# Optimization experiments

Hardware: AMD Instinct MI355X
Metric: run time of the kernel (lower is better)

The kernel has to match this reference:

```python
import jax, jax.numpy as jnp
import numpy as np

NEG_MASK = -9e15
ALPHA = 0.2  # LeakyReLU negative slope


def _gat_layer(h, adj, W, a):
    # h: [B,K,Fin], adj: [B,K,K], W: [Fin,F], a: [2F]
    Wh = jnp.einsum('bki,io->bko', h, W)            # [B,K,F]
    F = Wh.shape[-1]
    a_src, a_dst = a[:F], a[F:]
    # e_ij = LeakyReLU(a . [Wh_i || Wh_j]) = LeakyReLU(Wh_i.a_src + Wh_j.a_dst)
    f_src = Wh @ a_src                              # [B,K]
    f_dst = Wh @ a_dst                              # [B,K]
    e = jax.nn.leaky_relu(f_src[:, :, None] + f_dst[:, None, :], ALPHA)  # [B,K,K]
    e = jnp.where(adj > 0, e, NEG_MASK)
    att = jax.nn.softmax(e, axis=2)                 # softmax over neighbors j
    # dropout is identity in eval mode (training=False)
    h_prime = jnp.einsum('bkj,bjo->bko', att, Wh)   # [B,K,F]
    return jax.nn.elu(h_prime)


def setup_inputs() -> dict:
    key = jax.random.key(0)
    ks = jax.random.split(key, 6)
    B, K, Fin, H, Fout = 128, 512, 224, 64, 32
    x = jax.random.normal(ks[0], (B, K, Fin), dtype=jnp.float32)
    adj = jax.random.randint(ks[1], (B, K, K), 0, 2, dtype=jnp.int32)
    W1 = jax.random.normal(ks[2], (Fin, H), dtype=jnp.float32) * (1.0 / np.sqrt(Fin))
    a1 = jax.random.normal(ks[3], (2 * H,), dtype=jnp.float32) * 0.1
    W2 = jax.random.normal(ks[4], (H, Fout), dtype=jnp.float32) * (1.0 / np.sqrt(H))
    a2 = jax.random.normal(ks[5], (2 * Fout,), dtype=jnp.float32) * 0.1
    return {"x": x, "adj": adj, "W1": W1, "a1": a1, "W2": W2, "a2": a2}


def reference(x, adj, W1, a1, W2, a2):
    h = _gat_layer(x, adj, W1, a1)   # conv1: in -> hidden
    h = _gat_layer(h, adj, W2, a2)   # conv2: hidden -> out
    return h
```

## Files before the change

### kernel.cpp

```cpp
#include <hip/hip_runtime.h>
#include <stdint.h>


#define B_   128
#define K_   512
#define FIN  224
#define H1   64
#define H2   32

typedef float    f32x4 __attribute__((ext_vector_type(4)));
typedef short    s16x8 __attribute__((ext_vector_type(8)));
typedef unsigned short u16;

__device__ __forceinline__ u16 f2bf(float f){
  uint32_t u = __float_as_uint(f);
  u += 0x7FFFu + ((u >> 16) & 1u);
  return (u16)(u >> 16);
}
__device__ __forceinline__ float bf2f(u16 h){ return __uint_as_float(((uint32_t)h) << 16); }

__global__ __launch_bounds__(256) void k_bitmask(const int* __restrict__ adj, uint32_t* __restrict__ bits){
  size_t w = (size_t)blockIdx.x * 256 + threadIdx.x;
  const int4* p = reinterpret_cast<const int4*>(adj) + w * 8;
  uint32_t m = 0;
#pragma unroll
  for (int c = 0; c < 8; ++c){
    int4 v = p[c];
    m |= (v.x != 0 ? 1u : 0u) << (4*c + 0);
    m |= (v.y != 0 ? 1u : 0u) << (4*c + 1);
    m |= (v.z != 0 ? 1u : 0u) << (4*c + 2);
    m |= (v.w != 0 ? 1u : 0u) << (4*c + 3);
  }
  bits[w] = m;
}

__global__ __launch_bounds__(256) void k_prep(const float* __restrict__ W1, const float* __restrict__ W2,
                                              u16* __restrict__ W1b, u16* __restrict__ W2b){
  int t = blockIdx.x * 256 + threadIdx.x;
  if (t < FIN * H1) W1b[t] = f2bf(W1[t]);
  else { int u = t - FIN * H1; if (u < H1 * H2) W2b[u] = f2bf(W2[u]); }
}

template<int KD, int NO, bool AF32>
__global__ __launch_bounds__(256) void k_gemm(const void* __restrict__ Ain, const u16* __restrict__ Wb,
                                              const float* __restrict__ avec,
                                              u16* __restrict__ Whout, float* __restrict__ fs, float* __restrict__ fd){
  __shared__ u16 xs[64 * 40];
  __shared__ u16 wtT[NO * 56];
  const int tid  = threadIdx.x;
  const int wid  = tid >> 6, lane = tid & 63;
  const int g    = lane >> 4, lr = lane & 15;
  const size_t row0 = (size_t)blockIdx.x * 64;

  f32x4 acc[NO / 16];
#pragma unroll
  for (int c = 0; c < NO/16; ++c) acc[c] = (f32x4){0.f, 0.f, 0.f, 0.f};

  const int r_st = tid >> 2, c_st = tid & 3;
  const int j_w  = tid & 31, o0_w = (tid >> 5) * 8;

  for (int s = 0; s < KD/32; ++s){
    const int k0 = s * 32;
    __syncthreads();
    if (AF32){
      const float* A = (const float*)Ain;
      const float* src = A + (row0 + r_st) * KD + k0 + c_st * 8;
      float4 v0 = *(const float4*)(src);
      float4 v1 = *(const float4*)(src + 4);
      uint4 pk;
      pk.x = (uint32_t)f2bf(v0.x) | ((uint32_t)f2bf(v0.y) << 16);
      pk.y = (uint32_t)f2bf(v0.z) | ((uint32_t)f2bf(v0.w) << 16);
      pk.z = (uint32_t)f2bf(v1.x) | ((uint32_t)f2bf(v1.y) << 16);
      pk.w = (uint32_t)f2bf(v1.z) | ((uint32_t)f2bf(v1.w) << 16);
      *(uint4*)&xs[r_st * 40 + c_st * 8] = pk;
    } else {
      const u16* A = (const u16*)Ain;
      uint4 v = *(const uint4*)(A + (row0 + r_st) * KD + k0 + c_st * 8);
      *(uint4*)&xs[r_st * 40 + c_st * 8] = v;
    }
    if (tid < NO * 4){
      uint4 v = *(const uint4*)(Wb + (size_t)(k0 + j_w) * NO + o0_w);
      u16 h[8] = { (u16)(v.x & 0xFFFF), (u16)(v.x >> 16), (u16)(v.y & 0xFFFF), (u16)(v.y >> 16),
                   (u16)(v.z & 0xFFFF), (u16)(v.z >> 16), (u16)(v.w & 0xFFFF), (u16)(v.w >> 16) };
#pragma unroll
      for (int e = 0; e < 8; ++e) wtT[(o0_w + e) * 56 + j_w] = h[e];
    }
    __syncthreads();
    const s16x8 af = *(const s16x8*)&xs[(16 * wid + lr) * 40 + 8 * g];
#pragma unroll
    for (int c = 0; c < NO/16; ++c){
      const s16x8 bf = *(const s16x8*)&wtT[(16 * c + lr) * 56 + 8 * g];
      acc[c] = __builtin_amdgcn_mfma_f32_16x16x32_bf16(af, bf, acc[c], 0, 0, 0);
    }
  }

  float fsp[4] = {0.f,0.f,0.f,0.f}, fdp[4] = {0.f,0.f,0.f,0.f};
#pragma unroll
  for (int c = 0; c < NO/16; ++c){
    float as = avec[16 * c + lr], ad = avec[NO + 16 * c + lr];
#pragma unroll
    for (int r = 0; r < 4; ++r){
      fsp[r] += acc[c][r] * as;
      fdp[r] += acc[c][r] * ad;
      size_t row = row0 + 16 * wid + 4 * g + r;
      Whout[row * NO + 16 * c + lr] = f2bf(acc[c][r]);
    }
  }
#pragma unroll
  for (int m = 1; m < 16; m <<= 1){
#pragma unroll
    for (int r = 0; r < 4; ++r){ fsp[r] += __shfl_xor(fsp[r], m); fdp[r] += __shfl_xor(fdp[r], m); }
  }
  if (lr == 0){
#pragma unroll
    for (int r = 0; r < 4; ++r){
      size_t row = row0 + 16 * wid + 4 * g + r;
      fs[row] = fsp[r]; fd[row] = fdp[r];
    }
  }
}

template<int NO, bool OUTBF>
__global__ __launch_bounds__(256) void k_attn(const u16* __restrict__ Wh, const float* __restrict__ fsv,
                                              const float* __restrict__ fdv, const uint32_t* __restrict__ bits,
                                              void* __restrict__ outp){
  __shared__ u16  wtT[NO * 56];
  __shared__ float fd_s[K_];
  __shared__ float ls_s[64];
  const int tid = threadIdx.x;
  const int wid = tid >> 6, lane = tid & 63;
  const int g   = lane >> 4, lr = lane & 15;
  const int b   = blockIdx.x >> 3;
  const int i0  = (blockIdx.x & 7) * 64;
  const int prow = i0 + 16 * wid + lr;
  const float fsr = fsv[(size_t)b * K_ + prow];
  fd_s[tid]       = fdv[(size_t)b * K_ + tid];
  fd_s[256 + tid] = fdv[(size_t)b * K_ + 256 + tid];

  f32x4 acc[NO / 16];
#pragma unroll
  for (int c = 0; c < NO/16; ++c) acc[c] = (f32x4){0.f, 0.f, 0.f, 0.f};
  float lsum = 0.f;

  const uint32_t* brow = bits + ((size_t)b * K_ + prow) * 16;
  const int j_w = tid & 31, o0_w = (tid >> 5) * 8;

  for (int st = 0; st < 16; ++st){
    __syncthreads();
    if (tid < NO * 4){
      uint4 v = *(const uint4*)(Wh + ((size_t)b * K_ + st * 32 + j_w) * NO + o0_w);
      u16 h[8] = { (u16)(v.x & 0xFFFF), (u16)(v.x >> 16), (u16)(v.y & 0xFFFF), (u16)(v.y >> 16),
                   (u16)(v.z & 0xFFFF), (u16)(v.z >> 16), (u16)(v.w & 0xFFFF), (u16)(v.w >> 16) };
#pragma unroll
      for (int e = 0; e < 8; ++e) wtT[(o0_w + e) * 56 + j_w] = h[e];
    }
    uint32_t bw   = brow[st];
    uint32_t byte = (bw >> (8 * g)) & 0xFFu;
    float4 fd0 = *(const float4*)&fd_s[st * 32 + 8 * g];
    float4 fd1 = *(const float4*)&fd_s[st * 32 + 8 * g + 4];
    float pv[8] = { fd0.x, fd0.y, fd0.z, fd0.w, fd1.x, fd1.y, fd1.z, fd1.w };
    u16 ph[8];
    float lacc = 0.f;
#pragma unroll
    for (int e = 0; e < 8; ++e){
      float sc = fsr + pv[e];
      sc = fmaxf(sc, 0.2f * sc);
      float pe = __expf(sc - 8.0f);
      pe = ((byte >> e) & 1u) ? pe : 0.f;
      u16 h = f2bf(pe);
      ph[e] = h;
      lacc += bf2f(h);
    }
    lsum += lacc;
    s16x8 af;
    af[0]=(short)ph[0]; af[1]=(short)ph[1]; af[2]=(short)ph[2]; af[3]=(short)ph[3];
    af[4]=(short)ph[4]; af[5]=(short)ph[5]; af[6]=(short)ph[6]; af[7]=(short)ph[7];
    __syncthreads();
#pragma unroll
    for (int c = 0; c < NO/16; ++c){
      const s16x8 bf = *(const s16x8*)&wtT[(16 * c + lr) * 56 + 8 * g];
      acc[c] = __builtin_amdgcn_mfma_f32_16x16x32_bf16(af, bf, acc[c], 0, 0, 0);
    }
  }

  lsum += __shfl_xor(lsum, 16);
  lsum += __shfl_xor(lsum, 32);
  if (g == 0) ls_s[16 * wid + lr] = lsum;
  __syncthreads();

  float inv[4];
#pragma unroll
  for (int r = 0; r < 4; ++r) inv[r] = 1.0f / ls_s[16 * wid + 4 * g + r];
#pragma unroll
  for (int c = 0; c < NO/16; ++c){
#pragma unroll
    for (int r = 0; r < 4; ++r){
      float v = acc[c][r] * inv[r];
      v = v > 0.f ? v : (__expf(v) - 1.0f);
      size_t row = (size_t)b * K_ + i0 + 16 * wid + 4 * g + r;
      if (OUTBF) ((u16*)outp)[row * NO + 16 * c + lr] = f2bf(v);
      else       ((float*)outp)[row * NO + 16 * c + lr] = v;
    }
  }
}

extern "C" void kernel_launch(void* const* d_in, const int* in_sizes, int n_in,
                              void* d_out, int out_size, void* d_ws, size_t ws_size,
                              hipStream_t stream){
  const float* x   = (const float*)d_in[0];
  const int*   adj = (const int*)  d_in[1];
  const float* W1  = (const float*)d_in[2];
  const float* a1  = (const float*)d_in[3];
  const float* W2  = (const float*)d_in[4];
  const float* a2  = (const float*)d_in[5];
  float* out = (float*)d_out;

  char* ws = (char*)d_ws;
  u16*      Wh1  = (u16*)     (ws);
  u16*      h1   = (u16*)     (ws + 8388608);
  u16*      Wh2  = (u16*)     (ws + 16777216);
  uint32_t* bits = (uint32_t*)(ws + 20971520);
  float*    fs1  = (float*)   (ws + 25165824);
  float*    fd1  = (float*)   (ws + 25427968);
  float*    fs2  = (float*)   (ws + 25690112);
  float*    fd2  = (float*)   (ws + 25952256);
  u16*      W1b  = (u16*)     (ws + 26214400);
  u16*      W2b  = (u16*)     (ws + 26243072);

  k_bitmask<<<dim3(4096), dim3(256), 0, stream>>>(adj, bits);
  k_prep   <<<dim3(64),   dim3(256), 0, stream>>>(W1, W2, W1b, W2b);
  k_gemm<FIN, H1, true >  <<<dim3(1024), dim3(256), 0, stream>>>((const void*)x,  W1b, a1, Wh1, fs1, fd1);
  k_attn<H1, true >       <<<dim3(1024), dim3(256), 0, stream>>>(Wh1, fs1, fd1, bits, (void*)h1);
  k_gemm<H1,  H2, false>  <<<dim3(1024), dim3(256), 0, stream>>>((const void*)h1, W2b, a2, Wh2, fs2, fd2);
  k_attn<H2, false>       <<<dim3(1024), dim3(256), 0, stream>>>(Wh2, fs2, fd2, bits, (void*)out);
}
```

Baseline: 289.3 us.

## Store Wh transposed and feed MFMA operands straight from global memory

```diff
diff --git a/kernel.cpp b/kernel.cpp
--- a/kernel.cpp
+++ b/kernel.cpp
@@ -20,90 +20,74 @@
 __device__ __forceinline__ float bf2f(u16 h){ return __uint_as_float(((uint32_t)h) << 16); }
 
 __global__ __launch_bounds__(256) void k_bitmask(const int* __restrict__ adj, uint32_t* __restrict__ bits){
-  size_t w = (size_t)blockIdx.x * 256 + threadIdx.x;
-  const int4* p = reinterpret_cast<const int4*>(adj) + w * 8;
-  uint32_t m = 0;
-#pragma unroll
-  for (int c = 0; c < 8; ++c){
-    int4 v = p[c];
-    m |= (v.x != 0 ? 1u : 0u) << (4*c + 0);
-    m |= (v.y != 0 ? 1u : 0u) << (4*c + 1);
-    m |= (v.z != 0 ? 1u : 0u) << (4*c + 2);
-    m |= (v.w != 0 ? 1u : 0u) << (4*c + 3);
+  const int t = threadIdx.x, l = t & 63, w = t >> 6;
+  const int4* ap = reinterpret_cast<const int4*>(adj) + (size_t)blockIdx.x * 4096 + t;
+#pragma unroll 4
+  for (int it = 0; it < 16; ++it){
+    int4 v = ap[it * 256];
+    uint32_t nib = (v.x != 0 ? 1u : 0u) | (v.y != 0 ? 2u : 0u) | (v.z != 0 ? 4u : 0u) | (v.w != 0 ? 8u : 0u);
+    uint32_t val = nib << ((l & 7) * 4);
+    val |= __shfl_xor(val, 1);
+    val |= __shfl_xor(val, 2);
+    val |= __shfl_xor(val, 4);
+    if ((l & 7) == 0)
+      bits[(size_t)blockIdx.x * 512 + it * 32 + w * 8 + (l >> 3)] = val;
   }
-  bits[w] = m;
 }
 
 __global__ __launch_bounds__(256) void k_prep(const float* __restrict__ W1, const float* __restrict__ W2,
-                                              u16* __restrict__ W1b, u16* __restrict__ W2b){
+                                              u16* __restrict__ W1T, u16* __restrict__ W2T){
   int t = blockIdx.x * 256 + threadIdx.x;
-  if (t < FIN * H1) W1b[t] = f2bf(W1[t]);
-  else { int u = t - FIN * H1; if (u < H1 * H2) W2b[u] = f2bf(W2[u]); }
+  if (t < FIN * H1){ int k = t / H1, o = t % H1; W1T[o * FIN + k] = f2bf(W1[t]); }
+  else { int u = t - FIN * H1; if (u < H1 * H2){ int k = u / H2, o = u % H2; W2T[o * H1 + k] = f2bf(W2[u]); } }
 }
 
 template<int KD, int NO, bool AF32>
-__global__ __launch_bounds__(256) void k_gemm(const void* __restrict__ Ain, const u16* __restrict__ Wb,
+__global__ __launch_bounds__(256) void k_gemm(const void* __restrict__ Ain, const u16* __restrict__ WT,
                                               const float* __restrict__ avec,
-                                              u16* __restrict__ Whout, float* __restrict__ fs, float* __restrict__ fd){
-  __shared__ u16 xs[64 * 40];
-  __shared__ u16 wtT[NO * 56];
-  const int tid  = threadIdx.x;
-  const int wid  = tid >> 6, lane = tid & 63;
-  const int g    = lane >> 4, lr = lane & 15;
+                                              u16* __restrict__ WhT, float* __restrict__ fs, float* __restrict__ fd){
+  const int tid = threadIdx.x;
+  const int wid = tid >> 6, lane = tid & 63;
+  const int g = lane >> 4, lr = lane & 15;
   const size_t row0 = (size_t)blockIdx.x * 64;
+  const size_t arow = row0 + 16 * wid + lr;
 
   f32x4 acc[NO / 16];
 #pragma unroll
   for (int c = 0; c < NO/16; ++c) acc[c] = (f32x4){0.f, 0.f, 0.f, 0.f};
 
-  const int r_st = tid >> 2, c_st = tid & 3;
-  const int j_w  = tid & 31, o0_w = (tid >> 5) * 8;
-
-  for (int s = 0; s < KD/32; ++s){
-    const int k0 = s * 32;
-    __syncthreads();
+#pragma unroll
+  for (int s = 0; s < KD / 32; ++s){
+    const int k0 = s * 32 + 8 * g;
+    s16x8 af;
     if (AF32){
       const float* A = (const float*)Ain;
-      const float* src = A + (row0 + r_st) * KD + k0 + c_st * 8;
-      float4 v0 = *(const float4*)(src);
-      float4 v1 = *(const float4*)(src + 4);
-      uint4 pk;
-      pk.x = (uint32_t)f2bf(v0.x) | ((uint32_t)f2bf(v0.y) << 16);
-      pk.y = (uint32_t)f2bf(v0.z) | ((uint32_t)f2bf(v0.w) << 16);
-      pk.z = (uint32_t)f2bf(v1.x) | ((uint32_t)f2bf(v1.y) << 16);
-      pk.w = (uint32_t)f2bf(v1.z) | ((uint32_t)f2bf(v1.w) << 16);
-      *(uint4*)&xs[r_st * 40 + c_st * 8] = pk;
+      float4 v0 = *(const float4*)(A + arow * KD + k0);
+      float4 v1 = *(const float4*)(A + arow * KD + k0 + 4);
+      af[0] = (short)f2bf(v0.x); af[1] = (short)f2bf(v0.y); af[2] = (short)f2bf(v0.z); af[3] = (short)f2bf(v0.w);
+      af[4] = (short)f2bf(v1.x); af[5] = (short)f2bf(v1.y); af[6] = (short)f2bf(v1.z); af[7] = (short)f2bf(v1.w);
     } else {
-      const u16* A = (const u16*)Ain;
-      uint4 v = *(const uint4*)(A + (row0 + r_st) * KD + k0 + c_st * 8);
-      *(uint4*)&xs[r_st * 40 + c_st * 8] = v;
+      af = *(const s16x8*)((const u16*)Ain + arow * KD + k0);
     }
-    if (tid < NO * 4){
-      uint4 v = *(const uint4*)(Wb + (size_t)(k0 + j_w) * NO + o0_w);
-      u16 h[8] = { (u16)(v.x & 0xFFFF), (u16)(v.x >> 16), (u16)(v.y & 0xFFFF), (u16)(v.y >> 16),
-                   (u16)(v.z & 0xFFFF), (u16)(v.z >> 16), (u16)(v.w & 0xFFFF), (u16)(v.w >> 16) };
-#pragma unroll
-      for (int e = 0; e < 8; ++e) wtT[(o0_w + e) * 56 + j_w] = h[e];
-    }
-    __syncthreads();
-    const s16x8 af = *(const s16x8*)&xs[(16 * wid + lr) * 40 + 8 * g];
 #pragma unroll
     for (int c = 0; c < NO/16; ++c){
-      const s16x8 bf = *(const s16x8*)&wtT[(16 * c + lr) * 56 + 8 * g];
+      const s16x8 bf = *(const s16x8*)(WT + (size_t)(16 * c + lr) * KD + k0);
       acc[c] = __builtin_amdgcn_mfma_f32_16x16x32_bf16(af, bf, acc[c], 0, 0, 0);
     }
   }
 
+  const size_t b = row0 >> 9;
+  const int krow0 = (int)(row0 & 511) + 16 * wid + 4 * g;
   float fsp[4] = {0.f,0.f,0.f,0.f}, fdp[4] = {0.f,0.f,0.f,0.f};
 #pragma unroll
   for (int c = 0; c < NO/16; ++c){
-    float as = avec[16 * c + lr], ad = avec[NO + 16 * c + lr];
+    const int o = 16 * c + lr;
+    const float as = avec[o], ad = avec[NO + o];
 #pragma unroll
     for (int r = 0; r < 4; ++r){
       fsp[r] += acc[c][r] * as;
       fdp[r] += acc[c][r] * ad;
-      size_t row = row0 + 16 * wid + 4 * g + r;
-      Whout[row * NO + 16 * c + lr] = f2bf(acc[c][r]);
+      WhT[(b * NO + o) * K_ + krow0 + r] = f2bf(acc[c][r]);
     }
   }
 #pragma unroll
@@ -121,45 +105,32 @@
 }
 
 template<int NO, bool OUTBF>
-__global__ __launch_bounds__(256) void k_attn(const u16* __restrict__ Wh, const float* __restrict__ fsv,
+__global__ __launch_bounds__(256) void k_attn(const u16* __restrict__ WhT, const float* __restrict__ fsv,
                                               const float* __restrict__ fdv, const uint32_t* __restrict__ bits,
                                               void* __restrict__ outp){
-  __shared__ u16  wtT[NO * 56];
-  __shared__ float fd_s[K_];
-  __shared__ float ls_s[64];
   const int tid = threadIdx.x;
   const int wid = tid >> 6, lane = tid & 63;
-  const int g   = lane >> 4, lr = lane & 15;
-  const int b   = blockIdx.x >> 3;
-  const int i0  = (blockIdx.x & 7) * 64;
-  const int prow = i0 + 16 * wid + lr;
-  const float fsr = fsv[(size_t)b * K_ + prow];
-  fd_s[tid]       = fdv[(size_t)b * K_ + tid];
-  fd_s[256 + tid] = fdv[(size_t)b * K_ + 256 + tid];
+  const int g = lane >> 4, lr = lane & 15;
+  const int b = blockIdx.x >> 3;
+  const int i0 = (blockIdx.x & 7) * 64;
+  const int irow = i0 + 16 * wid + lr;
+  const float fsr = fsv[(size_t)b * K_ + irow];
+  const uint32_t* brow = bits + ((size_t)b * K_ + irow) * 16;
+  const float* fdb = fdv + (size_t)b * K_;
+  const u16* whb = WhT + (size_t)b * NO * K_;
 
   f32x4 acc[NO / 16];
 #pragma unroll
   for (int c = 0; c < NO/16; ++c) acc[c] = (f32x4){0.f, 0.f, 0.f, 0.f};
   float lsum = 0.f;
 
-  const uint32_t* brow = bits + ((size_t)b * K_ + prow) * 16;
-  const int j_w = tid & 31, o0_w = (tid >> 5) * 8;
-
   for (int st = 0; st < 16; ++st){
-    __syncthreads();
-    if (tid < NO * 4){
-      uint4 v = *(const uint4*)(Wh + ((size_t)b * K_ + st * 32 + j_w) * NO + o0_w);
-      u16 h[8] = { (u16)(v.x & 0xFFFF), (u16)(v.x >> 16), (u16)(v.y & 0xFFFF), (u16)(v.y >> 16),
-                   (u16)(v.z & 0xFFFF), (u16)(v.z >> 16), (u16)(v.w & 0xFFFF), (u16)(v.w >> 16) };
-#pragma unroll
-      for (int e = 0; e < 8; ++e) wtT[(o0_w + e) * 56 + j_w] = h[e];
-    }
-    uint32_t bw   = brow[st];
-    uint32_t byte = (bw >> (8 * g)) & 0xFFu;
-    float4 fd0 = *(const float4*)&fd_s[st * 32 + 8 * g];
-    float4 fd1 = *(const float4*)&fd_s[st * 32 + 8 * g + 4];
+    const int j0 = st * 32 + 8 * g;
+    const uint32_t byte = (brow[st] >> (8 * g)) & 0xFFu;
+    float4 fd0 = *(const float4*)(fdb + j0);
+    float4 fd1 = *(const float4*)(fdb + j0 + 4);
     float pv[8] = { fd0.x, fd0.y, fd0.z, fd0.w, fd1.x, fd1.y, fd1.z, fd1.w };
-    u16 ph[8];
+    s16x8 bp;
     float lacc = 0.f;
 #pragma unroll
     for (int e = 0; e < 8; ++e){
@@ -168,38 +139,30 @@
       float pe = __expf(sc - 8.0f);
       pe = ((byte >> e) & 1u) ? pe : 0.f;
       u16 h = f2bf(pe);
-      ph[e] = h;
+      bp[e] = (short)h;
       lacc += bf2f(h);
     }
     lsum += lacc;
-    s16x8 af;
-    af[0]=(short)ph[0]; af[1]=(short)ph[1]; af[2]=(short)ph[2]; af[3]=(short)ph[3];
-    af[4]=(short)ph[4]; af[5]=(short)ph[5]; af[6]=(short)ph[6]; af[7]=(short)ph[7];
-    __syncthreads();
 #pragma unroll
     for (int c = 0; c < NO/16; ++c){
-      const s16x8 bf = *(const s16x8*)&wtT[(16 * c + lr) * 56 + 8 * g];
-      acc[c] = __builtin_amdgcn_mfma_f32_16x16x32_bf16(af, bf, acc[c], 0, 0, 0);
+      const s16x8 aw = *(const s16x8*)(whb + (size_t)(16 * c + lr) * K_ + j0);
+      acc[c] = __builtin_amdgcn_mfma_f32_16x16x32_bf16(aw, bp, acc[c], 0, 0, 0);
     }
   }
 
   lsum += __shfl_xor(lsum, 16);
   lsum += __shfl_xor(lsum, 32);
-  if (g == 0) ls_s[16 * wid + lr] = lsum;
-  __syncthreads();
+  const float inv = 1.0f / lsum;
 
-  float inv[4];
-#pragma unroll
-  for (int r = 0; r < 4; ++r) inv[r] = 1.0f / ls_s[16 * wid + 4 * g + r];
 #pragma unroll
   for (int c = 0; c < NO/16; ++c){
 #pragma unroll
     for (int r = 0; r < 4; ++r){
-      float v = acc[c][r] * inv[r];
+      float v = acc[c][r] * inv;
       v = v > 0.f ? v : (__expf(v) - 1.0f);
-      size_t row = (size_t)b * K_ + i0 + 16 * wid + 4 * g + r;
-      if (OUTBF) ((u16*)outp)[row * NO + 16 * c + lr] = f2bf(v);
-      else       ((float*)outp)[row * NO + 16 * c + lr] = v;
+      const size_t idx = ((size_t)b * K_ + irow) * NO + 16 * c + 4 * g + r;
+      if (OUTBF) ((u16*)outp)[idx] = f2bf(v);
+      else       ((float*)outp)[idx] = v;
     }
   }
 }
@@ -216,21 +179,21 @@
   float* out = (float*)d_out;
 
   char* ws = (char*)d_ws;
-  u16*      Wh1  = (u16*)     (ws);
+  u16*      WhT1 = (u16*)     (ws);
   u16*      h1   = (u16*)     (ws + 8388608);
-  u16*      Wh2  = (u16*)     (ws + 16777216);
+  u16*      WhT2 = (u16*)     (ws + 16777216);
   uint32_t* bits = (uint32_t*)(ws + 20971520);
   float*    fs1  = (float*)   (ws + 25165824);
   float*    fd1  = (float*)   (ws + 25427968);
   float*    fs2  = (float*)   (ws + 25690112);
   float*    fd2  = (float*)   (ws + 25952256);
-  u16*      W1b  = (u16*)     (ws + 26214400);
-  u16*      W2b  = (u16*)     (ws + 26243072);
+  u16*      W1T  = (u16*)     (ws + 26214400);
+  u16*      W2T  = (u16*)     (ws + 26243072);
 
-  k_bitmask<<<dim3(4096), dim3(256), 0, stream>>>(adj, bits);
-  k_prep   <<<dim3(64),   dim3(256), 0, stream>>>(W1, W2, W1b, W2b);
-  k_gemm<FIN, H1, true >  <<<dim3(1024), dim3(256), 0, stream>>>((const void*)x,  W1b, a1, Wh1, fs1, fd1);
-  k_attn<H1, true >       <<<dim3(1024), dim3(256), 0, stream>>>(Wh1, fs1, fd1, bits, (void*)h1);
-  k_gemm<H1,  H2, false>  <<<dim3(1024), dim3(256), 0, stream>>>((const void*)h1, W2b, a2, Wh2, fs2, fd2);
-  k_attn<H2, false>       <<<dim3(1024), dim3(256), 0, stream>>>(Wh2, fs2, fd2, bits, (void*)out);
+  k_bitmask<<<dim3(2048), dim3(256), 0, stream>>>(adj, bits);
+  k_prep   <<<dim3(64),   dim3(256), 0, stream>>>(W1, W2, W1T, W2T);
+  k_gemm<FIN, H1, true >  <<<dim3(1024), dim3(256), 0, stream>>>((const void*)x,  W1T, a1, WhT1, fs1, fd1);
+  k_attn<H1, true >       <<<dim3(1024), dim3(256), 0, stream>>>(WhT1, fs1, fd1, bits, (void*)h1);
+  k_gemm<H1,  H2, false>  <<<dim3(1024), dim3(256), 0, stream>>>((const void*)h1, W2T, a2, WhT2, fs2, fd2);
+  k_attn<H2, false>       <<<dim3(1024), dim3(256), 0, stream>>>(WhT2, fs2, fd2, bits, (void*)out);
 }
```

New measurement: 325.2 us. 12.4% more time.
